# Kernel optimization log

Hardware: AMD Instinct MI355X
Metric: run time of the kernel (lower is better)

Reference implementation:

```python
import jax, jax.numpy as jnp
import numpy as np

B, T, D = 8, 4096, 1024
E, H = 8, 32  # n_experts, hidden_dim


def setup_inputs() -> dict:
    key = jax.random.key(0)
    ks = jax.random.split(key, 8)
    s = 1.0 / np.sqrt(D)
    sh = 1.0 / np.sqrt(H)
    return {
        "x": jax.random.normal(ks[0], (B, T, D), dtype=jnp.float32),
        "Wr": jax.random.uniform(ks[1], (D, E), jnp.float32, -s, s),
        "br": jax.random.uniform(ks[2], (E,), jnp.float32, -s, s),
        "W1": jax.random.uniform(ks[3], (E, D, 2 * H), jnp.float32, -s, s),
        "b1": jax.random.uniform(ks[4], (E, 2 * H), jnp.float32, -s, s),
        "W2": jax.random.uniform(ks[5], (E, H, D), jnp.float32, -sh, sh),
        "b2": jax.random.uniform(ks[6], (E, D), jnp.float32, -sh, sh),
    }


def reference(x, Wr, br, W1, b1, W2, b2):
    # Router: softmax gate over experts, [B,T,E]
    probs = jax.nn.softmax(x @ Wr + br, axis=-1)
    # All experts densely: h [B,E,T,2H]
    h = jnp.einsum('btd,edh->beth', x, W1) + b1[:, None, :]
    xp, gate = jnp.split(h, 2, axis=-1)  # chunk(2, dim=-1): first half value, second half gate
    act = xp * jax.nn.silu(gate)         # SwiGLU; dropout = identity (eval)
    out_e = jnp.einsum('beth,ehd->betd', act, W2) + b2[:, None, :]
    # Softmax-weighted sum over experts
    out = jnp.einsum('betd,bte->btd', out_e, probs)
    return out
```

## Files before the change

### kernel.cpp

```cpp
#include <hip/hip_runtime.h>

typedef float f32x4 __attribute__((ext_vector_type(4)));
typedef short bf16x8 __attribute__((ext_vector_type(8)));

#define B1S_KBSZ 67584
#define W2S_OFF  1081344
#define ACT_OFF  1736704

__device__ __forceinline__ unsigned short f2bf(float f) {
  unsigned int u = __float_as_uint(f);
  return (unsigned short)((u + 0x7FFFu + ((u >> 16) & 1u)) >> 16);
}
__device__ __forceinline__ unsigned int pack2(float a, float b) {
  return (unsigned int)f2bf(a) | ((unsigned int)f2bf(b) << 16);
}
__device__ __forceinline__ unsigned int cvtpk(float a, float b) {
  unsigned int r;
  asm("v_cvt_pk_bf16_f32 %0, %1, %2" : "=v"(r) : "v"(a), "v"(b));
  return r;
}
__device__ __forceinline__ bf16x8 cvt8(f32x4 lo, f32x4 hi) {
  union { uint4 u; bf16x8 b; } r;
  r.u.x = cvtpk(lo.x, lo.y); r.u.y = cvtpk(lo.z, lo.w);
  r.u.z = cvtpk(hi.x, hi.y); r.u.w = cvtpk(hi.z, hi.w);
  return r.b;
}
__device__ __forceinline__ void async16(const void* g, void* l) {
  __builtin_amdgcn_global_load_lds(
      (const __attribute__((address_space(1))) unsigned int*)g,
      (__attribute__((address_space(3))) unsigned int*)l, 16, 0, 0);
}

__global__ __launch_bounds__(256) void prep_all(const float* __restrict__ W1,
                                                const float* __restrict__ Wr,
                                                const float* __restrict__ W2,
                                                const float* __restrict__ b2,
                                                unsigned char* __restrict__ B1s,
                                                unsigned char* __restrict__ W2s) {
  if (blockIdx.x < 264) {
    int t = blockIdx.x * 256 + threadIdx.x;
    int c   = t & 7;
    int col = (t >> 3) % 528;
    int kb  = (t >> 3) / 528;
    int e   = col >> 6;
    int hh  = col & 63;
    float v[8];
    #pragma unroll
    for (int jj = 0; jj < 8; ++jj) {
      int k = kb * 64 + c * 8 + jj;
      float f;
      if (col < 512)      f = W1[(e * 1024 + k) * 64 + hh];
      else if (col < 520) f = Wr[k * 8 + (col - 512)];
      else                f = 0.0f;
      v[jj] = f;
    }
    *(uint4*)(B1s + kb * B1S_KBSZ + col * 128 + ((c ^ (col & 7)) * 16)) =
        make_uint4(pack2(v[0], v[1]), pack2(v[2], v[3]), pack2(v[4], v[5]), pack2(v[6], v[7]));
  } else {
    int t = (blockIdx.x - 264) * 256 + threadIdx.x;
    int cj  = t % 40;
    int col = t / 40;
    float v[8];
    #pragma unroll
    for (int jj = 0; jj < 8; ++jj) {
      int k = cj * 8 + jj;
      float f;
      if (k < 256)      f = W2[k * 1024 + col];
      else if (k < 264) f = b2[(k - 256) * 1024 + col];
      else              f = 0.0f;
      v[jj] = f;
    }
    int dstc = (cj & ~7) | ((cj & 7) ^ (col & 7));
    *(uint4*)(W2s + col * 640 + dstc * 16) =
        make_uint4(pack2(v[0], v[1]), pack2(v[2], v[3]), pack2(v[4], v[5]), pack2(v[6], v[7]));
  }
}

__global__ __launch_bounds__(256, 2) void moe_gemm1(
    const float* __restrict__ x, const float* __restrict__ br, const float* __restrict__ b1,
    const unsigned char* __restrict__ B1s, unsigned char* __restrict__ ACT) {
  __shared__ __align__(16) unsigned char smem[69632];

  const int tid  = threadIdx.x;
  const int lane = tid & 63;
  const int w    = tid >> 6;
  const int mg   = w >> 1;
  const int ng   = w & 1;
  const int f15  = lane & 15;
  const int fhi  = lane >> 4;
  const int k7   = f15 & 7;

  const int wid   = ((blockIdx.x & 7) << 8) + (blockIdx.x >> 3);
  const int mtile = wid >> 2;
  const int p     = wid & 3;
  const int m0    = mtile << 6;

  f32x4 acc[2][5];
  #pragma unroll
  for (int a = 0; a < 2; ++a)
    #pragma unroll
    for (int b = 0; b < 5; ++b) acc[a][b] = f32x4{0.f, 0.f, 0.f, 0.f};

  const float* xblk = x + (size_t)m0 * 1024;

  #define STAGE1(ks, buf)                                                        \
    { unsigned char* ab_ = smem + (buf) * 16384;                                 \
      unsigned char* bb_ = smem + 32768 + (buf) * 18432;                         \
      const float* xs_ = xblk + (ks) * 64;                                       \
      _Pragma("unroll")                                                          \
      for (int i = 0; i < 4; ++i) {                                              \
        int g = i * 256 + tid;                                                   \
        int row = g >> 4, cd = g & 15;                                           \
        async16(xs_ + (size_t)row * 1024 + ((cd ^ (row & 7)) << 2), ab_ + g * 16); \
      }                                                                          \
      const unsigned char* bsrc_ = B1s + (ks) * B1S_KBSZ;                        \
      _Pragma("unroll")                                                          \
      for (int i = 0; i < 5; ++i) {                                              \
        int g = i * 256 + tid;                                                   \
        if (g < 1152) {                                                          \
          int cf = g >> 7, r = (g >> 3) & 15, c = g & 7;                         \
          int col = (cf < 8) ? (p * 128 + cf * 16 + r) : (512 + r);              \
          async16(bsrc_ + col * 128 + c * 16, bb_ + g * 16);                     \
        }                                                                        \
      } }

  STAGE1(0, 0);
  __syncthreads();

  #pragma unroll 1
  for (int ks = 0; ks < 16; ++ks) {
    const int cur = ks & 1;
    if (ks < 15) STAGE1(ks + 1, cur ^ 1);
    const unsigned char* ab = smem + cur * 16384;
    const unsigned char* bb = smem + 32768 + cur * 18432;
    #pragma unroll
    for (int ksub = 0; ksub < 2; ++ksub) {
      const int ch = ((ksub * 4 + fhi) ^ k7) << 4;
      bf16x8 af[2];
      #pragma unroll
      for (int mf = 0; mf < 2; ++mf) {
        const int row = mg * 32 + mf * 16 + f15;
        const int cx  = ksub * 8 + fhi * 2;
        f32x4 lo = *(const f32x4*)(ab + row * 256 + (((cx)     ^ k7) << 4));
        f32x4 hi = *(const f32x4*)(ab + row * 256 + (((cx + 1) ^ k7) << 4));
        af[mf] = cvt8(lo, hi);
      }
      #pragma unroll
      for (int i = 0; i < 4; ++i) {
        bf16x8 bfr = *(const bf16x8*)(bb + (ng * 4 + i) * 2048 + f15 * 128 + ch);
        acc[0][i] = __builtin_amdgcn_mfma_f32_16x16x32_bf16(af[0], bfr, acc[0][i], 0, 0, 0);
        acc[1][i] = __builtin_amdgcn_mfma_f32_16x16x32_bf16(af[1], bfr, acc[1][i], 0, 0, 0);
      }
      if (ng == 0) {
        bf16x8 bfr = *(const bf16x8*)(bb + 8 * 2048 + f15 * 128 + ch);
        acc[0][4] = __builtin_amdgcn_mfma_f32_16x16x32_bf16(af[0], bfr, acc[0][4], 0, 0, 0);
        acc[1][4] = __builtin_amdgcn_mfma_f32_16x16x32_bf16(af[1], bfr, acc[1][4], 0, 0, 0);
      }
    }
    __syncthreads();
  }

  unsigned short* hb = (unsigned short*)smem;
  float* logit_lds   = (float*)(smem + 9216);
  unsigned short* pb = (unsigned short*)(smem + 11264);

  if (ng == 0 && f15 < 8) {
    float brv = br[f15];
    #pragma unroll
    for (int mf = 0; mf < 2; ++mf)
      #pragma unroll
      for (int r = 0; r < 4; ++r)
        logit_lds[(mg * 32 + mf * 16 + fhi * 4 + r) * 8 + f15] = acc[mf][4][r] + brv;
  }
  __syncthreads();

  const int e = p * 2 + ng;
  const float b1x0 = b1[e * 64 + f15],      b1x1 = b1[e * 64 + 16 + f15];
  const float b1g0 = b1[e * 64 + 32 + f15], b1g1 = b1[e * 64 + 48 + f15];

  #pragma unroll
  for (int mf = 0; mf < 2; ++mf) {
    #pragma unroll
    for (int r = 0; r < 4; ++r) {
      int row = mg * 32 + mf * 16 + fhi * 4 + r;
      const float* lg = logit_lds + row * 8;
      float l0 = lg[0], l1 = lg[1], l2 = lg[2], l3 = lg[3];
      float l4 = lg[4], l5 = lg[5], l6 = lg[6], l7 = lg[7];
      float mx = fmaxf(fmaxf(fmaxf(l0, l1), fmaxf(l2, l3)),
                       fmaxf(fmaxf(l4, l5), fmaxf(l6, l7)));
      float ssum = __expf(l0 - mx) + __expf(l1 - mx) + __expf(l2 - mx) + __expf(l3 - mx) +
                   __expf(l4 - mx) + __expf(l5 - mx) + __expf(l6 - mx) + __expf(l7 - mx);
      float rinv = 1.f / ssum;
      float pe = __expf(lg[e] - mx) * rinv;
      #pragma unroll
      for (int ci = 0; ci < 2; ++ci) {
        float xv = acc[mf][ci][r]     + (ci ? b1x1 : b1x0);
        float gv = acc[mf][ci + 2][r] + (ci ? b1g1 : b1g0);
        float av = pe * xv * gv / (1.f + __expf(-gv));
        hb[row * 72 + ng * 32 + ci * 16 + f15] = f2bf(av);
      }
      if (ng == 0 && f15 < 8) pb[row * 8 + f15] = f2bf(__expf(lg[f15] - mx) * rinv);
    }
  }
  __syncthreads();

  {
    const int row = tid >> 2, q = tid & 3, key = row & 7;
    unsigned char* arow = ACT + (size_t)(m0 + row) * 640;
    #pragma unroll
    for (int j = 0; j < 2; ++j) {
      int c = q * 2 + j;
      uint4 v = *(const uint4*)((const unsigned char*)hb + row * 144 + c * 16);
      *(uint4*)(arow + p * 128 + ((c ^ key) << 4)) = v;
    }
    if (p == 0) {
      #pragma unroll
      for (int j = 0; j < 2; ++j) {
        int c = q * 2 + j;
        uint4 v = make_uint4(0, 0, 0, 0);
        if (c == 0) v = *(const uint4*)((const unsigned char*)pb + row * 16);
        *(uint4*)(arow + 512 + ((c ^ key) << 4)) = v;
      }
    }
  }
}

__global__ __launch_bounds__(256, 3) void moe_gemm2(
    const unsigned char* __restrict__ ACT, const unsigned char* __restrict__ W2s,
    float* __restrict__ out) {
  __shared__ __align__(16) unsigned char smem[32768];
  const int tid  = threadIdx.x;
  const int lane = tid & 63;
  const int w    = tid >> 6;
  const int mg   = w >> 1, ng = w & 1;
  const int f15  = lane & 15, fhi = lane >> 4;
  const int k7   = f15 & 7;

  const int wid = ((blockIdx.x & 7) << 8) + (blockIdx.x >> 3);
  const int m0  = (wid >> 3) * 128;
  const int n0  = (wid & 7) * 128;

  f32x4 acc[4][4];
  #pragma unroll
  for (int a = 0; a < 4; ++a)
    #pragma unroll
    for (int b = 0; b < 4; ++b) acc[a][b] = f32x4{0.f, 0.f, 0.f, 0.f};

  const unsigned char* aB = ACT + (size_t)(m0 + mg * 64 + f15) * 640;
  const unsigned char* bB = W2s + (size_t)(n0 + ng * 64 + f15) * 640;
  const int ch0 = ((fhi)     ^ k7) << 4;
  const int ch1 = ((4 + fhi) ^ k7) << 4;

  #pragma unroll
  for (int kb = 0; kb < 5; ++kb) {
    bf16x8 a0[4], a1[4];
    #pragma unroll
    for (int mf = 0; mf < 4; ++mf) {
      const unsigned char* s_ = aB + mf * 10240 + kb * 128;
      a0[mf] = *(const bf16x8*)(s_ + ch0);
      a1[mf] = *(const bf16x8*)(s_ + ch1);
    }
    #pragma unroll
    for (int nf = 0; nf < 4; ++nf) {
      const unsigned char* s_ = bB + nf * 10240 + kb * 128;
      bf16x8 b0 = *(const bf16x8*)(s_ + ch0);
      bf16x8 b1v = *(const bf16x8*)(s_ + ch1);
      #pragma unroll
      for (int mf = 0; mf < 4; ++mf)
        acc[mf][nf] = __builtin_amdgcn_mfma_f32_16x16x32_bf16(a0[mf], b0, acc[mf][nf], 0, 0, 0);
      #pragma unroll
      for (int mf = 0; mf < 4; ++mf)
        acc[mf][nf] = __builtin_amdgcn_mfma_f32_16x16x32_bf16(a1[mf], b1v, acc[mf][nf], 0, 0, 0);
    }
  }

  float* slab = (float*)smem;
  #pragma unroll 1
  for (int q = 0; q < 2; ++q) {
    if (mg == q) {
      #pragma unroll
      for (int mf = 0; mf < 4; ++mf)
        #pragma unroll
        for (int nf = 0; nf < 4; ++nf)
          #pragma unroll
          for (int r = 0; r < 4; ++r) {
            int rl  = mf * 16 + fhi * 4 + r;
            int col = ng * 64 + nf * 16 + f15;
            slab[rl * 128 + (col ^ (((rl >> 2) & 7) << 2))] = acc[mf][nf][r];
          }
    }
    __syncthreads();
    #pragma unroll
    for (int j = 0; j < 8; ++j) {
      int rl = (tid >> 5) + j * 8;
      int c4 = tid & 31;
      f32x4 v = *(const f32x4*)(smem + rl * 512 + ((c4 ^ ((rl >> 2) & 7)) << 4));
      *(f32x4*)(out + (size_t)(m0 + q * 64 + rl) * 1024 + n0 + c4 * 4) = v;
    }
    __syncthreads();
  }
}

extern "C" void kernel_launch(void* const* d_in, const int* in_sizes, int n_in,
                              void* d_out, int out_size, void* d_ws, size_t ws_size,
                              hipStream_t stream) {
  const float* x  = (const float*)d_in[0];
  const float* Wr = (const float*)d_in[1];
  const float* br = (const float*)d_in[2];
  const float* W1 = (const float*)d_in[3];
  const float* b1 = (const float*)d_in[4];
  const float* W2 = (const float*)d_in[5];
  const float* b2 = (const float*)d_in[6];
  float* out = (float*)d_out;
  unsigned char* ws  = (unsigned char*)d_ws;
  unsigned char* B1s = ws;
  unsigned char* W2s = ws + W2S_OFF;
  unsigned char* ACT = ws + ACT_OFF;

  hipLaunchKernelGGL(prep_all, dim3(424), dim3(256), 0, stream, W1, Wr, W2, b2, B1s, W2s);
  hipLaunchKernelGGL(moe_gemm1, dim3(2048), dim3(256), 0, stream, x, br, b1, B1s, ACT);
  hipLaunchKernelGGL(moe_gemm2, dim3(2048), dim3(256), 0, stream, ACT, W2s, out);
}
```

Before: 155.4 us.

## Restructure gemm1 to one block per 64-row tile with direct global fragment loads

The first GEMM now launches one 512-thread block per 64-row tile of x, with each of the 8 waves computing one expert's 64 hidden columns, plus the router on the last wave. The old layout had four blocks per tile, each re-reading the same x rows. Operands are now loaded straight from global memory into registers, with no LDS double-buffering or per-step barriers. This cuts redundant x traffic fourfold and removes synchronisation, but relies on cache and latency hiding for uncoalesced 32-byte row loads. The router wave also carries extra MFMA work, which may cause imbalance.

```diff
diff --git a/kernel.cpp b/kernel.cpp
--- a/kernel.cpp
+++ b/kernel.cpp
@@ -24,11 +24,6 @@
   r.u.x = cvtpk(lo.x, lo.y); r.u.y = cvtpk(lo.z, lo.w);
   r.u.z = cvtpk(hi.x, hi.y); r.u.w = cvtpk(hi.z, hi.w);
   return r.b;
-}
-__device__ __forceinline__ void async16(const void* g, void* l) {
-  __builtin_amdgcn_global_load_lds(
-      (const __attribute__((address_space(1))) unsigned int*)g,
-      (__attribute__((address_space(3))) unsigned int*)l, 16, 0, 0);
 }
 
 __global__ __launch_bounds__(256) void prep_all(const float* __restrict__ W1,
@@ -76,151 +71,115 @@
   }
 }
 
-__global__ __launch_bounds__(256, 2) void moe_gemm1(
+__global__ __launch_bounds__(512, 2) void moe_gemm1(
     const float* __restrict__ x, const float* __restrict__ br, const float* __restrict__ b1,
     const unsigned char* __restrict__ B1s, unsigned char* __restrict__ ACT) {
-  __shared__ __align__(16) unsigned char smem[69632];
+  __shared__ __align__(16) unsigned char smem[35840];
 
   const int tid  = threadIdx.x;
   const int lane = tid & 63;
   const int w    = tid >> 6;
-  const int mg   = w >> 1;
-  const int ng   = w & 1;
   const int f15  = lane & 15;
   const int fhi  = lane >> 4;
   const int k7   = f15 & 7;
 
-  const int wid   = ((blockIdx.x & 7) << 8) + (blockIdx.x >> 3);
-  const int mtile = wid >> 2;
-  const int p     = wid & 3;
-  const int m0    = mtile << 6;
-
-  f32x4 acc[2][5];
-  #pragma unroll
-  for (int a = 0; a < 2; ++a)
-    #pragma unroll
-    for (int b = 0; b < 5; ++b) acc[a][b] = f32x4{0.f, 0.f, 0.f, 0.f};
-
-  const float* xblk = x + (size_t)m0 * 1024;
-
-  #define STAGE1(ks, buf)                                                        \
-    { unsigned char* ab_ = smem + (buf) * 16384;                                 \
-      unsigned char* bb_ = smem + 32768 + (buf) * 18432;                         \
-      const float* xs_ = xblk + (ks) * 64;                                       \
-      _Pragma("unroll")                                                          \
-      for (int i = 0; i < 4; ++i) {                                              \
-        int g = i * 256 + tid;                                                   \
-        int row = g >> 4, cd = g & 15;                                           \
-        async16(xs_ + (size_t)row * 1024 + ((cd ^ (row & 7)) << 2), ab_ + g * 16); \
-      }                                                                          \
-      const unsigned char* bsrc_ = B1s + (ks) * B1S_KBSZ;                        \
-      _Pragma("unroll")                                                          \
-      for (int i = 0; i < 5; ++i) {                                              \
-        int g = i * 256 + tid;                                                   \
-        if (g < 1152) {                                                          \
-          int cf = g >> 7, r = (g >> 3) & 15, c = g & 7;                         \
-          int col = (cf < 8) ? (p * 128 + cf * 16 + r) : (512 + r);              \
-          async16(bsrc_ + col * 128 + c * 16, bb_ + g * 16);                     \
-        }                                                                        \
-      } }
-
-  STAGE1(0, 0);
+  const int wid = ((blockIdx.x & 7) << 6) + (blockIdx.x >> 3);
+  const int m0  = wid << 6;
+
+  f32x4 acc[4][4];
+  f32x4 accR[4];
+  #pragma unroll
+  for (int a = 0; a < 4; ++a) {
+    #pragma unroll
+    for (int b = 0; b < 4; ++b) acc[a][b] = f32x4{0.f, 0.f, 0.f, 0.f};
+    accR[a] = f32x4{0.f, 0.f, 0.f, 0.f};
+  }
+
+  const float* xbase = x + (size_t)(m0 + f15) * 1024 + fhi * 8;
+  const unsigned char* bp  = B1s + (size_t)(w * 64 + f15) * 128;
+  const unsigned char* brt = B1s + (size_t)(512 + f15) * 128;
+  const bool rtr = (w == 7);
+
+  #pragma unroll
+  for (int ks = 0; ks < 16; ++ks) {
+    const size_t kso = (size_t)ks * B1S_KBSZ;
+    #pragma unroll
+    for (int ksub = 0; ksub < 2; ++ksub) {
+      bf16x8 af[4];
+      #pragma unroll
+      for (int mf = 0; mf < 4; ++mf) {
+        const float* s_ = xbase + mf * 16384 + ks * 64 + ksub * 32;
+        af[mf] = cvt8(*(const f32x4*)s_, *(const f32x4*)(s_ + 4));
+      }
+      const int ch = ((ksub * 4 + fhi) ^ k7) << 4;
+      bf16x8 bf[4];
+      #pragma unroll
+      for (int i = 0; i < 4; ++i) bf[i] = *(const bf16x8*)(bp + kso + i * 2048 + ch);
+      #pragma unroll
+      for (int i = 0; i < 4; ++i)
+        #pragma unroll
+        for (int mf = 0; mf < 4; ++mf)
+          acc[mf][i] = __builtin_amdgcn_mfma_f32_16x16x32_bf16(af[mf], bf[i], acc[mf][i], 0, 0, 0);
+      if (rtr) {
+        bf16x8 b4 = *(const bf16x8*)(brt + kso + ch);
+        #pragma unroll
+        for (int mf = 0; mf < 4; ++mf)
+          accR[mf] = __builtin_amdgcn_mfma_f32_16x16x32_bf16(af[mf], b4, accR[mf], 0, 0, 0);
+      }
+    }
+  }
+
+  unsigned short* hb = (unsigned short*)smem;
+  float* logit       = (float*)(smem + 33792);
+
+  if (rtr && f15 < 8) {
+    float brv = br[f15];
+    #pragma unroll
+    for (int mf = 0; mf < 4; ++mf)
+      #pragma unroll
+      for (int r = 0; r < 4; ++r)
+        logit[(mf * 16 + fhi * 4 + r) * 8 + f15] = accR[mf][r] + brv;
+  }
   __syncthreads();
 
-  #pragma unroll 1
-  for (int ks = 0; ks < 16; ++ks) {
-    const int cur = ks & 1;
-    if (ks < 15) STAGE1(ks + 1, cur ^ 1);
-    const unsigned char* ab = smem + cur * 16384;
-    const unsigned char* bb = smem + 32768 + cur * 18432;
-    #pragma unroll
-    for (int ksub = 0; ksub < 2; ++ksub) {
-      const int ch = ((ksub * 4 + fhi) ^ k7) << 4;
-      bf16x8 af[2];
-      #pragma unroll
-      for (int mf = 0; mf < 2; ++mf) {
-        const int row = mg * 32 + mf * 16 + f15;
-        const int cx  = ksub * 8 + fhi * 2;
-        f32x4 lo = *(const f32x4*)(ab + row * 256 + (((cx)     ^ k7) << 4));
-        f32x4 hi = *(const f32x4*)(ab + row * 256 + (((cx + 1) ^ k7) << 4));
-        af[mf] = cvt8(lo, hi);
-      }
-      #pragma unroll
-      for (int i = 0; i < 4; ++i) {
-        bf16x8 bfr = *(const bf16x8*)(bb + (ng * 4 + i) * 2048 + f15 * 128 + ch);
-        acc[0][i] = __builtin_amdgcn_mfma_f32_16x16x32_bf16(af[0], bfr, acc[0][i], 0, 0, 0);
-        acc[1][i] = __builtin_amdgcn_mfma_f32_16x16x32_bf16(af[1], bfr, acc[1][i], 0, 0, 0);
-      }
-      if (ng == 0) {
-        bf16x8 bfr = *(const bf16x8*)(bb + 8 * 2048 + f15 * 128 + ch);
-        acc[0][4] = __builtin_amdgcn_mfma_f32_16x16x32_bf16(af[0], bfr, acc[0][4], 0, 0, 0);
-        acc[1][4] = __builtin_amdgcn_mfma_f32_16x16x32_bf16(af[1], bfr, acc[1][4], 0, 0, 0);
-      }
-    }
-    __syncthreads();
-  }
-
-  unsigned short* hb = (unsigned short*)smem;
-  float* logit_lds   = (float*)(smem + 9216);
-  unsigned short* pb = (unsigned short*)(smem + 11264);
-
-  if (ng == 0 && f15 < 8) {
-    float brv = br[f15];
-    #pragma unroll
-    for (int mf = 0; mf < 2; ++mf)
-      #pragma unroll
-      for (int r = 0; r < 4; ++r)
-        logit_lds[(mg * 32 + mf * 16 + fhi * 4 + r) * 8 + f15] = acc[mf][4][r] + brv;
-  }
-  __syncthreads();
-
-  const int e = p * 2 + ng;
+  const int e = w;
   const float b1x0 = b1[e * 64 + f15],      b1x1 = b1[e * 64 + 16 + f15];
   const float b1g0 = b1[e * 64 + 32 + f15], b1g1 = b1[e * 64 + 48 + f15];
 
   #pragma unroll
-  for (int mf = 0; mf < 2; ++mf) {
+  for (int mf = 0; mf < 4; ++mf) {
     #pragma unroll
     for (int r = 0; r < 4; ++r) {
-      int row = mg * 32 + mf * 16 + fhi * 4 + r;
-      const float* lg = logit_lds + row * 8;
+      int row = mf * 16 + fhi * 4 + r;
+      const float* lg = logit + row * 8;
       float l0 = lg[0], l1 = lg[1], l2 = lg[2], l3 = lg[3];
       float l4 = lg[4], l5 = lg[5], l6 = lg[6], l7 = lg[7];
       float mx = fmaxf(fmaxf(fmaxf(l0, l1), fmaxf(l2, l3)),
                        fmaxf(fmaxf(l4, l5), fmaxf(l6, l7)));
       float ssum = __expf(l0 - mx) + __expf(l1 - mx) + __expf(l2 - mx) + __expf(l3 - mx) +
                    __expf(l4 - mx) + __expf(l5 - mx) + __expf(l6 - mx) + __expf(l7 - mx);
-      float rinv = 1.f / ssum;
-      float pe = __expf(lg[e] - mx) * rinv;
+      float pe = __expf(lg[e] - mx) / ssum;
       #pragma unroll
       for (int ci = 0; ci < 2; ++ci) {
         float xv = acc[mf][ci][r]     + (ci ? b1x1 : b1x0);
         float gv = acc[mf][ci + 2][r] + (ci ? b1g1 : b1g0);
         float av = pe * xv * gv / (1.f + __expf(-gv));
-        hb[row * 72 + ng * 32 + ci * 16 + f15] = f2bf(av);
+        hb[row * 264 + e * 32 + ci * 16 + f15] = f2bf(av);
       }
-      if (ng == 0 && f15 < 8) pb[row * 8 + f15] = f2bf(__expf(lg[f15] - mx) * rinv);
+      if (f15 == 0) hb[row * 264 + 256 + e] = f2bf(pe);
     }
   }
   __syncthreads();
 
   {
-    const int row = tid >> 2, q = tid & 3, key = row & 7;
+    const int row = tid >> 3, q = tid & 7, key = row & 7;
     unsigned char* arow = ACT + (size_t)(m0 + row) * 640;
     #pragma unroll
-    for (int j = 0; j < 2; ++j) {
-      int c = q * 2 + j;
-      uint4 v = *(const uint4*)((const unsigned char*)hb + row * 144 + c * 16);
-      *(uint4*)(arow + p * 128 + ((c ^ key) << 4)) = v;
-    }
-    if (p == 0) {
-      #pragma unroll
-      for (int j = 0; j < 2; ++j) {
-        int c = q * 2 + j;
-        uint4 v = make_uint4(0, 0, 0, 0);
-        if (c == 0) v = *(const uint4*)((const unsigned char*)pb + row * 16);
-        *(uint4*)(arow + 512 + ((c ^ key) << 4)) = v;
-      }
+    for (int j = 0; j < 5; ++j) {
+      int c = q + j * 8;
+      uint4 v = make_uint4(0, 0, 0, 0);
+      if (c <= 32) v = *(const uint4*)((const unsigned char*)hb + row * 528 + c * 16);
+      *(uint4*)(arow + (c >> 3) * 128 + (((c & 7) ^ key) << 4)) = v;
     }
   }
 }
@@ -318,6 +277,6 @@
   unsigned char* ACT = ws + ACT_OFF;
 
   hipLaunchKernelGGL(prep_all, dim3(424), dim3(256), 0, stream, W1, Wr, W2, b2, B1s, W2s);
-  hipLaunchKernelGGL(moe_gemm1, dim3(2048), dim3(256), 0, stream, x, br, b1, B1s, ACT);
+  hipLaunchKernelGGL(moe_gemm1, dim3(512), dim3(512), 0, stream, x, br, b1, B1s, ACT);
   hipLaunchKernelGGL(moe_gemm2, dim3(2048), dim3(256), 0, stream, ACT, W2s, out);
 }
```

Measured after the change: 224.4 us. 44.4% more time.
